# Performance work log

Measured on AMD Instinct MI355X. Metric: run time of the kernel, lower is better.

## Reference

```python
import jax, jax.numpy as jnp
import numpy as np

N = 100_000      # nodes
E = 1_600_000    # edges
NG = 512         # graphs in batch
EPS = 1e-5


def _prop(x, src, dst, n, add_self_loops):
    """GCN-normalized sparse propagation: agg_i = sum_{j->i} d_j^-1/2 d_i^-1/2 x_j."""
    ones = jnp.ones(src.shape[0], x.dtype)
    deg = jax.ops.segment_sum(ones, dst, num_segments=n)
    if add_self_loops:
        deg = deg + 1.0
    dinv = jnp.where(deg > 0, jax.lax.rsqrt(jnp.maximum(deg, 1e-12)), 0.0)
    w = dinv[src] * dinv[dst]                       # [E]
    agg = jax.ops.segment_sum(x[src] * w[:, None], dst, num_segments=n)
    if add_self_loops:
        agg = agg + x * (dinv * dinv)[:, None]
    return agg


def setup_inputs() -> dict:
    key = jax.random.key(0)
    ks = jax.random.split(key, 24)
    w = lambda k, s: jax.random.normal(k, s, jnp.float32) * 0.05
    dim = 100
    return {
        "x": jax.random.normal(ks[0], (N, 128), jnp.float32),
        "src": jax.random.randint(ks[1], (E,), 0, N),
        "dst": jax.random.randint(ks[2], (E,), 0, N),
        "batch": jnp.sort(jax.random.randint(ks[3], (N,), 0, NG)),
        # SGConv 1 & 2 (propagate then Linear)
        "W1": w(ks[4], (128, dim)), "b1": jnp.zeros((dim,), jnp.float32),
        "W2": w(ks[5], (dim, dim)), "b2": jnp.zeros((dim,), jnp.float32),
        # BatchNorm1d affine params
        "gamma": jnp.ones((dim,), jnp.float32), "beta": jnp.zeros((dim,), jnp.float32),
        # ARMAConv (num_stacks=1, num_layers=1)
        "Wa_init": w(ks[6], (dim, dim)), "Wa_root": w(ks[7], (dim, dim)),
        "ba": jnp.zeros((dim,), jnp.float32),
        # MLP head
        "Wf1": w(ks[8], (dim, 2 * dim)), "bf1": jnp.zeros((2 * dim,), jnp.float32),
        "Wf2": w(ks[9], (2 * dim, 3 * dim)), "bf2": jnp.zeros((3 * dim,), jnp.float32),
        "Wf3": w(ks[10], (3 * dim, 2 * dim)), "bf3": jnp.zeros((2 * dim,), jnp.float32),
        "Wf4": w(ks[11], (2 * dim, 1)), "bf4": jnp.zeros((1,), jnp.float32),
    }


def reference(x, src, dst, batch, W1, b1, W2, b2, gamma, beta,
              Wa_init, Wa_root, ba, Wf1, bf1, Wf2, bf2, Wf3, bf3, Wf4, bf4):
    n = x.shape[0]
    # SGConv (K=1): propagate with self-loop gcn_norm, then linear; ReLU
    h = jax.nn.relu(_prop(x, src, dst, n, True) @ W1 + b1)
    h = jax.nn.relu(_prop(h, src, dst, n, True) @ W2 + b2)
    # BatchNorm1d (training mode: batch statistics, biased var)
    mu = jnp.mean(h, axis=0)
    var = jnp.mean((h - mu) ** 2, axis=0)
    h = (h - mu) * jax.lax.rsqrt(var + EPS) * gamma + beta
    # ARMAConv (1 stack, 1 layer): ReLU(A_hat (h W_init) + h W_root + b), no self-loops
    a = jax.nn.relu(_prop(h @ Wa_init, src, dst, n, False) + h @ Wa_root + ba)
    # global_add_pool over graph ids
    g = jax.ops.segment_sum(a, batch, num_segments=NG)   # [NG, dim]
    # MLP head
    g = jax.nn.relu(g @ Wf1 + bf1)
    g = jax.nn.relu(g @ Wf2 + bf2)
    g = jax.nn.relu(g @ Wf3 + bf3)
    return g @ Wf4 + bf4
```

## Files before the change

kernel.cpp:

```cpp
#include <hip/hip_runtime.h>
#include <hip/hip_fp16.h>

#define NNODES 100000
#define NEDGES 1600000
#define NGRAPH 512
#define DIM    100
#define DP     128
#define EPSBN  1e-5f
#define NBUK   ((NNODES + 255) >> 8)
#define BINCH  2048

typedef _Float16 half8 __attribute__((ext_vector_type(8)));
typedef float floatx4 __attribute__((ext_vector_type(4)));

__global__ __launch_bounds__(512) void bin_count_kernel(const int* __restrict__ dst,
                                                        int* __restrict__ btotal, int e) {
    __shared__ int lc[NBUK];
    int tid = threadIdx.x;
    int base = blockIdx.x * BINCH;
    int m = e - base; if (m > BINCH) m = BINCH;
    for (int b = tid; b < NBUK; b += 512) lc[b] = 0;
    __syncthreads();
    for (int j = tid; j < m; j += 512)
        atomicAdd(&lc[dst[base + j] >> 8], 1);
    __syncthreads();
    for (int b = tid; b < NBUK; b += 512)
        if (lc[b]) atomicAdd(&btotal[b], lc[b]);
}

__global__ void bucket_scan_kernel(const int* __restrict__ btotal, int* __restrict__ bbase,
                                   int* __restrict__ bcursor, int e,
                                   const int* __restrict__ batch, int* __restrict__ gstart, int n) {
    __shared__ int s[512];
    int tid = threadIdx.x;
    int v = (tid < NBUK) ? btotal[tid] : 0;
    s[tid] = v; __syncthreads();
    for (int o = 1; o < 512; o <<= 1) {
        int t = (tid >= o) ? s[tid - o] : 0;
        __syncthreads();
        s[tid] += t;
        __syncthreads();
    }
    if (tid < NBUK) {
        int base = s[tid] - v;
        bbase[tid] = base;
        bcursor[tid] = base;
    }
    if (tid == 0) bbase[NBUK] = e;

    {
        int g = tid;
        int lo = 0, hi = n;
        while (lo < hi) {
            int mid = (lo + hi) >> 1;
            if (batch[mid] < g) lo = mid + 1; else hi = mid;
        }
        gstart[g] = lo;
        if (g == 0) gstart[NGRAPH] = n;
    }
}

__global__ __launch_bounds__(512) void bin_kernel(
        const int* __restrict__ src, const int* __restrict__ dst,
        int* __restrict__ bcursor, unsigned int* __restrict__ gpairs, int e) {
    __shared__ int2 lpairs[BINCH];
    __shared__ int lcount[NBUK], lstart[NBUK], lcur[NBUK], gbase[NBUK];
    __shared__ int s[512];
    int tid = threadIdx.x;
    int base = blockIdx.x * BINCH;
    int m = e - base; if (m > BINCH) m = BINCH;

    for (int b = tid; b < NBUK; b += 512) lcount[b] = 0;
    __syncthreads();
    for (int j = tid; j < m; j += 512)
        atomicAdd(&lcount[dst[base + j] >> 8], 1);
    __syncthreads();

    int v = (tid < NBUK) ? lcount[tid] : 0;
    s[tid] = v; __syncthreads();
    for (int o = 1; o < 512; o <<= 1) {
        int t = (tid >= o) ? s[tid - o] : 0;
        __syncthreads();
        s[tid] += t;
        __syncthreads();
    }
    if (tid < NBUK) {
        lstart[tid] = s[tid] - v;
        lcur[tid] = s[tid] - v;
        gbase[tid] = atomicAdd(&bcursor[tid], v);
    }
    __syncthreads();

    for (int j = tid; j < m; j += 512) {
        int sv = src[base + j], d = dst[base + j];
        int p = atomicAdd(&lcur[d >> 8], 1);
        lpairs[p] = make_int2(sv, d);
    }
    __syncthreads();
    for (int j = tid; j < m; j += 512) {
        int2 pr = lpairs[j];
        int b = pr.y >> 8;
        gpairs[gbase[b] + (j - lstart[b])] =
            ((unsigned int)pr.x << 8) | ((unsigned int)pr.y & 255u);
    }
}

__global__ __launch_bounds__(256) void bucket_build_kernel(
        const unsigned int* __restrict__ gpairs, const int* __restrict__ bbase,
        int* __restrict__ off, int* __restrict__ ssorted,
        float* __restrict__ dsl, float* __restrict__ dnsl, int n, int e) {
    __shared__ int cnt[256];
    __shared__ int sc[256];
    int b = blockIdx.x, tid = threadIdx.x;
    int node0 = b << 8;
    int e0 = bbase[b], e1 = bbase[b + 1];

    cnt[tid] = 0;
    __syncthreads();
    for (int j = e0 + tid; j < e1; j += 256)
        atomicAdd(&cnt[gpairs[j] & 255u], 1);
    __syncthreads();

    int c = cnt[tid];
    sc[tid] = c; __syncthreads();
    for (int o = 1; o < 256; o <<= 1) {
        int t = (tid >= o) ? sc[tid - o] : 0;
        __syncthreads();
        sc[tid] += t;
        __syncthreads();
    }
    int excl = sc[tid] - c;

    int node = node0 + tid;
    if (node < n) {
        off[node] = e0 + excl;
        float cf = (float)c;
        dsl[node] = rsqrtf(cf + 1.0f);
        dnsl[node] = (c > 0) ? rsqrtf(cf) : 0.0f;
    }
    if (b == NBUK - 1 && tid == 0) off[n] = e;

    __syncthreads();
    cnt[tid] = e0 + excl;
    __syncthreads();
    for (int j = e0 + tid; j < e1; j += 256) {
        unsigned int pk = gpairs[j];
        int p = atomicAdd(&cnt[pk & 255u], 1);
        ssorted[p] = (int)(pk >> 8);
    }
}

__global__ void packW4_kernel(const float* __restrict__ W1, const float* __restrict__ W2,
                              const float* __restrict__ W3, const float* __restrict__ W4,
                              _Float16* __restrict__ Wt1, _Float16* __restrict__ Wt2,
                              _Float16* __restrict__ Wt3, _Float16* __restrict__ Wt4,
                              const float* __restrict__ b1, const float* __restrict__ b2,
                              float* __restrict__ b1p, float* __restrict__ b2p,
                              int* __restrict__ btotal, float* __restrict__ bnsum,
                              float* __restrict__ bnsq, __half* __restrict__ buf0zr) {
    if (blockIdx.x == 256) {
        int t = threadIdx.x;
        if (t < 128) {
            b1p[t] = (t < DIM) ? b1[t] : 0.f;
            b2p[t] = (t < DIM) ? b2[t] : 0.f;
            bnsum[t] = 0.f;
            bnsq[t] = 0.f;
        }
        for (int i = t; i < NBUK; i += 256) btotal[i] = 0;
        if (t < 64) ((unsigned int*)buf0zr)[t] = 0u;
        return;
    }
    int which = blockIdx.x >> 6;
    int idx = (blockIdx.x & 63) * 256 + threadIdx.x;
    const float* W = (which == 0) ? W1 : (which == 1) ? W2 : (which == 2) ? W3 : W4;
    _Float16* Wt  = (which == 0) ? Wt1 : (which == 1) ? Wt2 : (which == 2) ? Wt3 : Wt4;
    int K = (which == 0) ? 128 : DIM;
    int j = idx & 7;
    int l = (idx >> 3) & 63;
    int c = idx >> 9;
    int t = c >> 2, k0 = c & 3;
    int nn = t * 16 + (l & 15);
    int k = k0 * 32 + (l >> 4) * 8 + j;
    float v = (k < K && nn < DIM) ? W[k * DIM + nn] : 0.f;
    Wt[idx] = (_Float16)v;
}

__global__ __launch_bounds__(256) void prop_kernel(
        const __half* __restrict__ pre, const int* __restrict__ ssorted,
        const int* __restrict__ off, const float* __restrict__ dinv,
        const float* __restrict__ bias, __half* __restrict__ outH, int n) {
    int wave = (blockIdx.x * blockDim.x + threadIdx.x) >> 6;
    int lane = threadIdx.x & 63;
    if (wave >= n) return;
    int e0 = off[wave], e1 = off[wave + 1];
    int deg = e1 - e0;
    int g = lane >> 4;
    int q = lane & 15;
    const int ZR = n;

    float acc[8];
#pragma unroll
    for (int i = 0; i < 8; i++) acc[i] = 0.f;

    auto addu = [&](uint4 u) {
        float2 f;
        f = __half22float2(*(__half2*)&u.x); acc[0] += f.x; acc[1] += f.y;
        f = __half22float2(*(__half2*)&u.y); acc[2] += f.x; acc[3] += f.y;
        f = __half22float2(*(__half2*)&u.z); acc[4] += f.x; acc[5] += f.y;
        f = __half22float2(*(__half2*)&u.w); acc[6] += f.x; acc[7] += f.y;
    };
    auto rowptr = [&](int s) -> const uint4* {
        return (const uint4*)&pre[(long)s * DP + q * 8];
    };

    for (int base = 0; base < deg; base += 64) {
        int m = deg - base; if (m > 64) m = 64;
        int sidx = (lane < m) ? ssorted[e0 + base + lane] : ZR;
        for (int j = 0; j < m; j += 16) {
            int s0 = __shfl(sidx, j + g);
            int s1 = __shfl(sidx, j + 4 + g);
            int s2 = __shfl(sidx, j + 8 + g);
            int s3 = __shfl(sidx, j + 12 + g);
            uint4 u0 = *rowptr(s0);
            uint4 u1 = *rowptr(s1);
            uint4 u2 = *rowptr(s2);
            uint4 u3 = *rowptr(s3);
            addu(u0); addu(u1); addu(u2); addu(u3);
        }
    }

#pragma unroll
    for (int i = 0; i < 8; i++) {
        acc[i] += __shfl_xor(acc[i], 16);
        acc[i] += __shfl_xor(acc[i], 32);
    }

    if (g == 0) {
        float dn = dinv[wave];
        addu(*rowptr(wave));
        float4 b0 = *(const float4*)&bias[q * 8];
        float4 b1v = *(const float4*)&bias[q * 8 + 4];
        float o[8];
        o[0] = fmaxf(dn * acc[0] + b0.x, 0.f);
        o[1] = fmaxf(dn * acc[1] + b0.y, 0.f);
        o[2] = fmaxf(dn * acc[2] + b0.z, 0.f);
        o[3] = fmaxf(dn * acc[3] + b0.w, 0.f);
        o[4] = fmaxf(dn * acc[4] + b1v.x, 0.f);
        o[5] = fmaxf(dn * acc[5] + b1v.y, 0.f);
        o[6] = fmaxf(dn * acc[6] + b1v.z, 0.f);
        o[7] = fmaxf(dn * acc[7] + b1v.w, 0.f);
        __half2 p0 = __floats2half2_rn(o[0], o[1]);
        __half2 p1 = __floats2half2_rn(o[2], o[3]);
        __half2 p2 = __floats2half2_rn(o[4], o[5]);
        __half2 p3 = __floats2half2_rn(o[6], o[7]);
        uint4 u;
        u.x = *(unsigned int*)&p0;
        u.y = *(unsigned int*)&p1;
        u.z = *(unsigned int*)&p2;
        u.w = *(unsigned int*)&p3;
        *(uint4*)&outH[(long)wave * DP + q * 8] = u;
    }
}

__global__ __launch_bounds__(256) void prop_arma_kernel(
        const __half* __restrict__ pre, const int* __restrict__ ssorted,
        const int* __restrict__ off, const float* __restrict__ dinv,
        const __half* __restrict__ R, __half* __restrict__ outH, int n) {
    int wave = (blockIdx.x * blockDim.x + threadIdx.x) >> 6;
    int lane = threadIdx.x & 63;
    if (wave >= n) return;
    int e0 = off[wave], e1 = off[wave + 1];
    int deg = e1 - e0;
    int g = lane >> 4;
    int q = lane & 15;
    const int ZR = n;

    float acc[8];
#pragma unroll
    for (int i = 0; i < 8; i++) acc[i] = 0.f;

    auto addu = [&](uint4 u) {
        float2 f;
        f = __half22float2(*(__half2*)&u.x); acc[0] += f.x; acc[1] += f.y;
        f = __half22float2(*(__half2*)&u.y); acc[2] += f.x; acc[3] += f.y;
        f = __half22float2(*(__half2*)&u.z); acc[4] += f.x; acc[5] += f.y;
        f = __half22float2(*(__half2*)&u.w); acc[6] += f.x; acc[7] += f.y;
    };
    auto rowptr = [&](int s) -> const uint4* {
        return (const uint4*)&pre[(long)s * DP + q * 8];
    };

    for (int base = 0; base < deg; base += 64) {
        int m = deg - base; if (m > 64) m = 64;
        int sidx = (lane < m) ? ssorted[e0 + base + lane] : ZR;
        for (int j = 0; j < m; j += 16) {
            int s0 = __shfl(sidx, j + g);
            int s1 = __shfl(sidx, j + 4 + g);
            int s2 = __shfl(sidx, j + 8 + g);
            int s3 = __shfl(sidx, j + 12 + g);
            uint4 u0 = *rowptr(s0);
            uint4 u1 = *rowptr(s1);
            uint4 u2 = *rowptr(s2);
            uint4 u3 = *rowptr(s3);
            addu(u0); addu(u1); addu(u2); addu(u3);
        }
    }

#pragma unroll
    for (int i = 0; i < 8; i++) {
        acc[i] += __shfl_xor(acc[i], 16);
        acc[i] += __shfl_xor(acc[i], 32);
    }

    if (g == 0) {
        float dn = dinv[wave];
        uint4 r4 = *(const uint4*)&R[(long)wave * DP + q * 8];
        float rr[8];
        float2 f;
        f = __half22float2(*(__half2*)&r4.x); rr[0] = f.x; rr[1] = f.y;
        f = __half22float2(*(__half2*)&r4.y); rr[2] = f.x; rr[3] = f.y;
        f = __half22float2(*(__half2*)&r4.z); rr[4] = f.x; rr[5] = f.y;
        f = __half22float2(*(__half2*)&r4.w); rr[6] = f.x; rr[7] = f.y;
        float o[8];
#pragma unroll
        for (int i = 0; i < 8; i++) o[i] = fmaxf(dn * acc[i] + rr[i], 0.f);
        __half2 p0 = __floats2half2_rn(o[0], o[1]);
        __half2 p1 = __floats2half2_rn(o[2], o[3]);
        __half2 p2 = __floats2half2_rn(o[4], o[5]);
        __half2 p3 = __floats2half2_rn(o[6], o[7]);
        uint4 u;
        u.x = *(unsigned int*)&p0;
        u.y = *(unsigned int*)&p1;
        u.z = *(unsigned int*)&p2;
        u.w = *(unsigned int*)&p3;
        *(uint4*)&outH[(long)wave * DP + q * 8] = u;
    }
}

__global__ __launch_bounds__(256) void matmul_a32_kernel(
        const float* __restrict__ A, const _Float16* __restrict__ WtF,
        const float* __restrict__ rowscale, __half* __restrict__ Ch, int M) {
    __shared__ char smraw[64 * 132 * 4];
    _Float16* Bs = (_Float16*)smraw;
    float* Ct = (float*)smraw;
    int tid = threadIdx.x;
    int wave = tid >> 6;
    int lane = tid & 63;
    int m16 = lane & 15;
    int quad = lane >> 4;
    long row0blk = (long)blockIdx.x * 128;

    {
        const uint4* s = (const uint4*)WtF;
        uint4* d = (uint4*)Bs;
        for (int i = tid; i < 2048; i += 256) d[i] = s[i];
    }

    half8 af[2][4];
#pragma unroll
    for (int t = 0; t < 2; t++) {
        long ar = row0blk + t * 64 + wave * 16 + m16; if (ar >= M) ar = M - 1;
        const float* Ap = &A[ar * DP + quad * 8];
#pragma unroll
        for (int k0 = 0; k0 < 4; k0++) {
            float4 v0 = *(const float4*)(Ap + k0 * 32);
            float4 v1 = *(const float4*)(Ap + k0 * 32 + 4);
            half8 o;
            o[0] = (_Float16)v0.x; o[1] = (_Float16)v0.y;
            o[2] = (_Float16)v0.z; o[3] = (_Float16)v0.w;
            o[4] = (_Float16)v1.x; o[5] = (_Float16)v1.y;
            o[6] = (_Float16)v1.z; o[7] = (_Float16)v1.w;
            af[t][k0] = o;
        }
    }
    __syncthreads();

    floatx4 acc[2][8];
#pragma unroll
    for (int t = 0; t < 2; t++)
#pragma unroll
        for (int a = 0; a < 8; a++) acc[t][a] = (floatx4){0.f, 0.f, 0.f, 0.f};

#pragma unroll
    for (int c = 0; c < 32; c++) {
        half8 bf = *(const half8*)&Bs[(c * 64 + lane) * 8];
        acc[0][c >> 2] = __builtin_amdgcn_mfma_f32_16x16x32_f16(af[0][c & 3], bf, acc[0][c >> 2], 0, 0, 0);
        acc[1][c >> 2] = __builtin_amdgcn_mfma_f32_16x16x32_f16(af[1][c & 3], bf, acc[1][c >> 2], 0, 0, 0);
    }

    int lrow0 = wave * 16 + quad * 4;
#pragma unroll
    for (int t = 0; t < 2; t++) {
        __syncthreads();
#pragma unroll
        for (int a = 0; a < 8; a++)
#pragma unroll
            for (int r = 0; r < 4; r++)
                Ct[(lrow0 + r) * 132 + a * 16 + m16] = acc[t][a][r];
        __syncthreads();
        for (int idx = tid; idx < 64 * 32; idx += 256) {
            int lr = idx >> 5, c4 = idx & 31;
            long grow = row0blk + t * 64 + lr;
            if (grow >= M) continue;
            int col = c4 * 4;
            float4 v = *(const float4*)&Ct[lr * 132 + col];
            float rs = rowscale[grow];
            v.x *= rs; v.y *= rs; v.z *= rs; v.w *= rs;
            __half2 p01 = __floats2half2_rn(v.x, v.y);
            __half2 p23 = __floats2half2_rn(v.z, v.w);
            uint2 u;
            u.x = *(unsigned int*)&p01;
            u.y = *(unsigned int*)&p23;
            *(uint2*)&Ch[grow * DP + col] = u;
        }
    }
}

__global__ __launch_bounds__(256) void matmul_a16_kernel(
        const __half* __restrict__ A, const _Float16* __restrict__ WtF,
        const float* __restrict__ rowscale, __half* __restrict__ Ch, int M) {
    __shared__ char smraw[64 * 132 * 4];
    _Float16* Bs = (_Float16*)smraw;
    float* Ct = (float*)smraw;
    int tid = threadIdx.x;
    int wave = tid >> 6;
    int lane = tid & 63;
    int m16 = lane & 15;
    int quad = lane >> 4;
    long row0blk = (long)blockIdx.x * 128;

    {
        const uint4* s = (const uint4*)WtF;
        uint4* d = (uint4*)Bs;
        for (int i = tid; i < 2048; i += 256) d[i] = s[i];
    }

    half8 af[2][4];
#pragma unroll
    for (int t = 0; t < 2; t++) {
        long ar = row0blk + t * 64 + wave * 16 + m16; if (ar >= M) ar = M - 1;
        const _Float16* Ap = (const _Float16*)&A[ar * DP + quad * 8];
#pragma unroll
        for (int k0 = 0; k0 < 4; k0++)
            af[t][k0] = *(const half8*)(Ap + k0 * 32);
    }
    __syncthreads();

    floatx4 acc[2][8];
#pragma unroll
    for (int t = 0; t < 2; t++)
#pragma unroll
        for (int a = 0; a < 8; a++) acc[t][a] = (floatx4){0.f, 0.f, 0.f, 0.f};

#pragma unroll
    for (int c = 0; c < 32; c++) {
        half8 bf = *(const half8*)&Bs[(c * 64 + lane) * 8];
        acc[0][c >> 2] = __builtin_amdgcn_mfma_f32_16x16x32_f16(af[0][c & 3], bf, acc[0][c >> 2], 0, 0, 0);
        acc[1][c >> 2] = __builtin_amdgcn_mfma_f32_16x16x32_f16(af[1][c & 3], bf, acc[1][c >> 2], 0, 0, 0);
    }

    int lrow0 = wave * 16 + quad * 4;
#pragma unroll
    for (int t = 0; t < 2; t++) {
        __syncthreads();
#pragma unroll
        for (int a = 0; a < 8; a++)
#pragma unroll
            for (int r = 0; r < 4; r++)
                Ct[(lrow0 + r) * 132 + a * 16 + m16] = acc[t][a][r];
        __syncthreads();
        for (int idx = tid; idx < 64 * 32; idx += 256) {
            int lr = idx >> 5, c4 = idx & 31;
            long grow = row0blk + t * 64 + lr;
            if (grow >= M) continue;
            int col = c4 * 4;
            float4 v = *(const float4*)&Ct[lr * 132 + col];
            float rs = rowscale[grow];
            v.x *= rs; v.y *= rs; v.z *= rs; v.w *= rs;
            __half2 p01 = __floats2half2_rn(v.x, v.y);
            __half2 p23 = __floats2half2_rn(v.z, v.w);
            uint2 u;
            u.x = *(unsigned int*)&p01;
            u.y = *(unsigned int*)&p23;
            *(uint2*)&Ch[grow * DP + col] = u;
        }
    }
}

__global__ __launch_bounds__(256) void matmul_dual_kernel(
        const __half* __restrict__ A, const _Float16* __restrict__ WtF3,
        const _Float16* __restrict__ WtF4, const float* __restrict__ ba,
        const float* __restrict__ rowscale,
        const float* __restrict__ bnscale, const float* __restrict__ bnshift,
        __half* __restrict__ Ch1, __half* __restrict__ ChR, int M, int Kout) {
    __shared__ char smraw[64 * 132 * 4];
    _Float16* Bs = (_Float16*)smraw;
    float* Ct = (float*)smraw;
    int tid = threadIdx.x;
    int wave = tid >> 6;
    int lane = tid & 63;
    int m16 = lane & 15;
    int quad = lane >> 4;
    long row0blk = (long)blockIdx.x * 64;
    long row0 = row0blk + wave * 16;

    half8 af[4];
    {
        long ar = row0 + m16; if (ar >= M) ar = M - 1;
        const _Float16* Ap = (const _Float16*)&A[ar * DP + quad * 8];
#pragma unroll
        for (int k0 = 0; k0 < 4; k0++) {
            half8 h = *(const half8*)(Ap + k0 * 32);
            int c0 = quad * 8 + k0 * 32;
            float4 sc0 = *(const float4*)&bnscale[c0];
            float4 sc1 = *(const float4*)&bnscale[c0 + 4];
            float4 sh0 = *(const float4*)&bnshift[c0];
            float4 sh1 = *(const float4*)&bnshift[c0 + 4];
            half8 o;
            o[0] = (_Float16)((float)h[0] * sc0.x + sh0.x);
            o[1] = (_Float16)((float)h[1] * sc0.y + sh0.y);
            o[2] = (_Float16)((float)h[2] * sc0.z + sh0.z);
            o[3] = (_Float16)((float)h[3] * sc0.w + sh0.w);
            o[4] = (_Float16)((float)h[4] * sc1.x + sh1.x);
            o[5] = (_Float16)((float)h[5] * sc1.y + sh1.y);
            o[6] = (_Float16)((float)h[6] * sc1.z + sh1.z);
            o[7] = (_Float16)((float)h[7] * sc1.w + sh1.w);
            af[k0] = o;
        }
    }

    floatx4 acc3[8], acc4[8];
#pragma unroll
    for (int t = 0; t < 8; t++) {
        acc3[t] = (floatx4){0.f, 0.f, 0.f, 0.f};
        acc4[t] = (floatx4){0.f, 0.f, 0.f, 0.f};
    }

    {
        const uint4* s = (const uint4*)WtF3;
        uint4* d = (uint4*)Bs;
        for (int i = tid; i < 2048; i += 256) d[i] = s[i];
    }
    __syncthreads();
#pragma unroll
    for (int c = 0; c < 32; c++) {
        half8 bf = *(const half8*)&Bs[(c * 64 + lane) * 8];
        acc3[c >> 2] = __builtin_amdgcn_mfma_f32_16x16x32_f16(af[c & 3], bf, acc3[c >> 2], 0, 0, 0);
    }
    __syncthreads();

    {
        const uint4* s = (const uint4*)WtF4;
        uint4* d = (uint4*)Bs;
        for (int i = tid; i < 2048; i += 256) d[i] = s[i];
    }
    __syncthreads();
#pragma unroll
    for (int c = 0; c < 32; c++) {
        half8 bf = *(const half8*)&Bs[(c * 64 + lane) * 8];
        acc4[c >> 2] = __builtin_amdgcn_mfma_f32_16x16x32_f16(af[c & 3], bf, acc4[c >> 2], 0, 0, 0);
    }
    __syncthreads();

    int lrow0 = wave * 16 + quad * 4;

#pragma unroll
    for (int t = 0; t < 8; t++)
#pragma unroll
        for (int r = 0; r < 4; r++)
            Ct[(lrow0 + r) * 132 + t * 16 + m16] = acc3[t][r];
    __syncthreads();
    for (int idx = tid; idx < 64 * 32; idx += 256) {
        int lr = idx >> 5, c4 = idx & 31;
        long grow = row0blk + lr;
        if (grow >= M) continue;
        int col = c4 * 4;
        float4 v = *(const float4*)&Ct[lr * 132 + col];
        float rs = rowscale[grow];
        v.x *= rs; v.y *= rs; v.z *= rs; v.w *= rs;
        __half2 p01 = __floats2half2_rn(v.x, v.y);
        __half2 p23 = __floats2half2_rn(v.z, v.w);
        uint2 u;
        u.x = *(unsigned int*)&p01;
        u.y = *(unsigned int*)&p23;
        *(uint2*)&Ch1[grow * DP + col] = u;
    }
    __syncthreads();

#pragma unroll
    for (int t = 0; t < 8; t++)
#pragma unroll
        for (int r = 0; r < 4; r++)
            Ct[(lrow0 + r) * 132 + t * 16 + m16] = acc4[t][r];
    __syncthreads();
    for (int idx = tid; idx < 64 * 32; idx += 256) {
        int lr = idx >> 5, c4 = idx & 31;
        long grow = row0blk + lr;
        if (grow >= M) continue;
        int col = c4 * 4;
        float4 v = *(const float4*)&Ct[lr * 132 + col];
        if (col + 4 <= Kout) {
            float4 bb = *(const float4*)&ba[col];
            v.x += bb.x; v.y += bb.y; v.z += bb.z; v.w += bb.w;
        }
        __half2 p01 = __floats2half2_rn(v.x, v.y);
        __half2 p23 = __floats2half2_rn(v.z, v.w);
        uint2 u;
        u.x = *(unsigned int*)&p01;
        u.y = *(unsigned int*)&p23;
        *(uint2*)&ChR[grow * DP + col] = u;
    }
}

__global__ __launch_bounds__(512) void bnstats_kernel(const __half* __restrict__ h,
                                                      float* __restrict__ bnsum,
                                                      float* __restrict__ bnsq, int n) {
    __shared__ float2 sred[512], qred[512];
    int tid = threadIdx.x;
    int col2 = tid & 63;
    int rgrp = tid >> 6;
    float2 s = make_float2(0.f, 0.f), qv = make_float2(0.f, 0.f);
    if (col2 < 52) {
        for (int r = blockIdx.x * 8 + rgrp; r < n; r += gridDim.x * 8) {
            __half2 hv = *(const __half2*)&h[(long)r * DP + col2 * 2];
            float2 f = __half22float2(hv);
            s.x += f.x; s.y += f.y;
            qv.x += f.x * f.x; qv.y += f.y * f.y;
        }
    }
    sred[tid] = s; qred[tid] = qv;
    __syncthreads();
    if (tid < 52) {
        float2 ts = make_float2(0.f, 0.f), tq = make_float2(0.f, 0.f);
#pragma unroll
        for (int gg = 0; gg < 8; gg++) {
            float2 v = sred[gg * 64 + tid]; ts.x += v.x; ts.y += v.y;
            v = qred[gg * 64 + tid]; tq.x += v.x; tq.y += v.y;
        }
        atomicAdd(&bnsum[tid * 2], ts.x);
        atomicAdd(&bnsum[tid * 2 + 1], ts.y);
        atomicAdd(&bnsq[tid * 2], tq.x);
        atomicAdd(&bnsq[tid * 2 + 1], tq.y);
    }
}

__global__ void bn_prep_kernel(const float* __restrict__ sum, const float* __restrict__ sq,
                               const float* __restrict__ gamma, const float* __restrict__ beta,
                               float* __restrict__ scale, float* __restrict__ shift, int n) {
    int c = threadIdx.x;
    float sc = 0.f, sh = 0.f;
    if (c < DIM) {
        float inv_n = 1.0f / (float)n;
        float mu = sum[c] * inv_n;
        float var = sq[c] * inv_n - mu * mu;
        float rs = rsqrtf(var + EPSBN);
        sc = rs * gamma[c];
        sh = beta[c] - mu * sc;
    }
    scale[c] = sc;
    shift[c] = sh;
}

__global__ __launch_bounds__(512) void pmlp_kernel(
        const __half* __restrict__ a, const int* __restrict__ gstart,
        const float* __restrict__ Wf1, const float* __restrict__ bf1,
        const float* __restrict__ Wf2, const float* __restrict__ bf2,
        const float* __restrict__ Wf3, const float* __restrict__ bf3,
        const float* __restrict__ Wf4, const float* __restrict__ bf4,
        float* __restrict__ out) {
    __shared__ float2 red[512];
    __shared__ float gsum[128], a1[200], a2[300], a3[200], red1[512];
    int b = blockIdx.x, tid = threadIdx.x;

    {
        int col2 = tid & 63;
        int rgrp = tid >> 6;
        int lo = gstart[b], hi = gstart[b + 1];
        float2 s = make_float2(0.f, 0.f);
        for (int r = lo + rgrp; r < hi; r += 8) {
            __half2 h = *(const __half2*)&a[(long)r * DP + col2 * 2];
            float2 f = __half22float2(h);
            s.x += f.x; s.y += f.y;
        }
        red[tid] = s;
        __syncthreads();
        if (tid < 64) {
            float2 t = make_float2(0.f, 0.f);
#pragma unroll
            for (int gg = 0; gg < 8; gg++) {
                float2 v = red[gg * 64 + tid];
                t.x += v.x; t.y += v.y;
            }
            gsum[tid * 2] = t.x;
            gsum[tid * 2 + 1] = t.y;
        }
        __syncthreads();
    }

    for (int c = tid; c < 200; c += 512) {
        float s = bf1[c];
        for (int k = 0; k < 100; k++) s += gsum[k] * Wf1[k * 200 + c];
        a1[c] = fmaxf(s, 0.f);
    }
    __syncthreads();
    for (int c = tid; c < 300; c += 512) {
        float s = bf2[c];
        for (int k = 0; k < 200; k++) s += a1[k] * Wf2[k * 300 + c];
        a2[c] = fmaxf(s, 0.f);
    }
    __syncthreads();
    for (int c = tid; c < 200; c += 512) {
        float s = bf3[c];
        for (int k = 0; k < 300; k++) s += a2[k] * Wf3[k * 200 + c];
        a3[c] = fmaxf(s, 0.f);
    }
    __syncthreads();
    red1[tid] = (tid < 200) ? a3[tid] * Wf4[tid] : 0.f;
    __syncthreads();
    for (int o = 256; o > 0; o >>= 1) {
        if (tid < o) red1[tid] += red1[tid + o];
        __syncthreads();
    }
    if (tid == 0) out[b] = red1[0] + bf4[0];
}

extern "C" void kernel_launch(void* const* d_in, const int* in_sizes, int n_in,
                              void* d_out, int out_size, void* d_ws, size_t ws_size,
                              hipStream_t stream) {
    const float* x      = (const float*)d_in[0];
    const int*   src    = (const int*)d_in[1];
    const int*   dst    = (const int*)d_in[2];
    const int*   batch  = (const int*)d_in[3];
    const float* W1     = (const float*)d_in[4];
    const float* b1     = (const float*)d_in[5];
    const float* W2     = (const float*)d_in[6];
    const float* b2     = (const float*)d_in[7];
    const float* gamma  = (const float*)d_in[8];
    const float* beta   = (const float*)d_in[9];
    const float* Wa_init= (const float*)d_in[10];
    const float* Wa_root= (const float*)d_in[11];
    const float* ba     = (const float*)d_in[12];
    const float* Wf1    = (const float*)d_in[13];
    const float* bf1    = (const float*)d_in[14];
    const float* Wf2    = (const float*)d_in[15];
    const float* bf2    = (const float*)d_in[16];
    const float* Wf3    = (const float*)d_in[17];
    const float* bf3    = (const float*)d_in[18];
    const float* Wf4    = (const float*)d_in[19];
    const float* bf4    = (const float*)d_in[20];
    float* out = (float*)d_out;

    const int n = NNODES;
    const int e = NEDGES;

    char* ws = (char*)d_ws;
    auto carve = [&](size_t bytes) -> void* {
        void* p = (void*)ws;
        ws += (bytes + 255) & ~(size_t)255;
        return p;
    };
    __half* buf0    = (__half*)carve((size_t)(n + 1) * DP * 2);
    __half* buf1    = (__half*)carve((size_t)n * DP * 2);
    __half* bufR    = (__half*)carve((size_t)n * DP * 2);
    __half* bufC    = (__half*)carve((size_t)n * DP * 2);
    _Float16* Wt1   = (_Float16*)carve((size_t)DP * DP * 2);
    _Float16* Wt2   = (_Float16*)carve((size_t)DP * DP * 2);
    _Float16* Wt3   = (_Float16*)carve((size_t)DP * DP * 2);
    _Float16* Wt4   = (_Float16*)carve((size_t)DP * DP * 2);
    int*    off     = (int*)carve((size_t)(n + 1) * 4);
    int*    btotal  = (int*)carve((size_t)NBUK * 4);
    int*    bbase   = (int*)carve((size_t)(NBUK + 1) * 4);
    int*    bcursor = (int*)carve((size_t)NBUK * 4);
    int*    ssorted = (int*)carve((size_t)e * 4);
    unsigned int* gpairs = (unsigned int*)carve((size_t)e * 4);
    float*  dinv_sl = (float*)carve((size_t)n * 4);
    float*  dinv_nsl= (float*)carve((size_t)n * 4);
    float*  bnsum   = (float*)carve(DP * 4);
    float*  bnsq    = (float*)carve(DP * 4);
    float*  bnscale = (float*)carve(DP * 4);
    float*  bnshift = (float*)carve(DP * 4);
    float*  b1p     = (float*)carve(DP * 4);
    float*  b2p     = (float*)carve(DP * 4);
    int*    gstart  = (int*)carve((size_t)(NGRAPH + 1) * 4);

    const int nchunk = (e + BINCH - 1) / BINCH;

    packW4_kernel<<<257, 256, 0, stream>>>(W1, W2, Wa_init, Wa_root, Wt1, Wt2, Wt3, Wt4,
                                           b1, b2, b1p, b2p, btotal, bnsum, bnsq,
                                           buf0 + (size_t)n * DP);

    bin_count_kernel<<<nchunk, 512, 0, stream>>>(dst, btotal, e);
    bucket_scan_kernel<<<1, 512, 0, stream>>>(btotal, bbase, bcursor, e, batch, gstart, n);
    bin_kernel<<<nchunk, 512, 0, stream>>>(src, dst, bcursor, gpairs, e);
    bucket_build_kernel<<<NBUK, 256, 0, stream>>>(gpairs, bbase, off, ssorted, dinv_sl, dinv_nsl, n, e);

    const int prop_blocks = (n + 3) / 4;
    const int mm_blocks128 = (n + 127) / 128;
    const int mm_blocks64 = (n + 63) / 64;

    matmul_a32_kernel<<<mm_blocks128, 256, 0, stream>>>(x, Wt1, dinv_sl, buf0, n);
    prop_kernel<<<prop_blocks, 256, 0, stream>>>(buf0, ssorted, off, dinv_sl, b1p, buf1, n);

    matmul_a16_kernel<<<mm_blocks128, 256, 0, stream>>>(buf1, Wt2, dinv_sl, buf0, n);
    prop_kernel<<<prop_blocks, 256, 0, stream>>>(buf0, ssorted, off, dinv_sl, b2p, buf1, n);

    bnstats_kernel<<<512, 512, 0, stream>>>(buf1, bnsum, bnsq, n);
    bn_prep_kernel<<<1, 128, 0, stream>>>(bnsum, bnsq, gamma, beta, bnscale, bnshift, n);

    matmul_dual_kernel<<<mm_blocks64, 256, 0, stream>>>(buf1, Wt3, Wt4, ba, dinv_nsl, bnscale, bnshift, buf0, bufR, n, DIM);
    prop_arma_kernel<<<prop_blocks, 256, 0, stream>>>(buf0, ssorted, off, dinv_nsl, bufR, bufC, n);

    pmlp_kernel<<<NGRAPH, 512, 0, stream>>>(bufC, gstart, Wf1, bf1, Wf2, bf2, Wf3, bf3, Wf4, bf4, out);
}
```

Before: 504.5 us.

## Slice propagation features into per-XCD column slabs with work-stealing queues

The pre-propagation matmul output now goes into 7 column slices of 16 halves each, rather than a 128-wide padded row layout. The three propagation kernels are merged into one persistent kernel. Each block picks a slice based on its XCC id and pulls 128-node chunks from an atomic queue, stealing from other slices once its own queue is empty. The aim is to keep each slice's 3.2MB gather footprint resident in one XCD's L2 and to stop gathering padded columns, at the cost of atomic queue traffic and the assumption that there are 7-8 XCDs.

```diff
diff --git a/kernel.cpp b/kernel.cpp
--- a/kernel.cpp
+++ b/kernel.cpp
@@ -6,12 +6,17 @@
 #define NGRAPH 512
 #define DIM    100
 #define DP     128
+#define SLICES 7
 #define EPSBN  1e-5f
 #define NBUK   ((NNODES + 255) >> 8)
 #define BINCH  2048
+#define PERW   32
+#define NCH    128
+#define QPAD   32
 
 typedef _Float16 half8 __attribute__((ext_vector_type(8)));
 typedef float floatx4 __attribute__((ext_vector_type(4)));
+
 
 __global__ __launch_bounds__(512) void bin_count_kernel(const int* __restrict__ dst,
                                                         int* __restrict__ btotal, int e) {
@@ -157,7 +162,8 @@
                               const float* __restrict__ b1, const float* __restrict__ b2,
                               float* __restrict__ b1p, float* __restrict__ b2p,
                               int* __restrict__ btotal, float* __restrict__ bnsum,
-                              float* __restrict__ bnsq, __half* __restrict__ buf0zr) {
+                              float* __restrict__ bnsq, __half* __restrict__ buf0,
+                              int* __restrict__ qcur, int n) {
     if (blockIdx.x == 256) {
         int t = threadIdx.x;
         if (t < 128) {
@@ -167,7 +173,11 @@
             bnsq[t] = 0.f;
         }
         for (int i = t; i < NBUK; i += 256) btotal[i] = 0;
-        if (t < 64) ((unsigned int*)buf0zr)[t] = 0u;
+        for (int i = t; i < 3 * SLICES * QPAD; i += 256) qcur[i] = 0;
+        if (t < SLICES * 8) {
+            int sl = t >> 3, wd = t & 7;
+            ((unsigned int*)buf0)[((size_t)sl * (n + 1) + n) * 8 + wd] = 0u;
+        }
         return;
     }
     int which = blockIdx.x >> 6;
@@ -185,155 +195,148 @@
     Wt[idx] = (_Float16)v;
 }
 
-__global__ __launch_bounds__(256) void prop_kernel(
-        const __half* __restrict__ pre, const int* __restrict__ ssorted,
+__global__ __launch_bounds__(256) void prop_slice_kernel(
+        const __half* __restrict__ T, const int* __restrict__ ssorted,
         const int* __restrict__ off, const float* __restrict__ dinv,
-        const float* __restrict__ bias, __half* __restrict__ outH, int n) {
-    int wave = (blockIdx.x * blockDim.x + threadIdx.x) >> 6;
-    int lane = threadIdx.x & 63;
-    if (wave >= n) return;
-    int e0 = off[wave], e1 = off[wave + 1];
-    int deg = e1 - e0;
-    int g = lane >> 4;
-    int q = lane & 15;
+        const float* __restrict__ bias, const __half* __restrict__ R,
+        __half* __restrict__ outH, int* __restrict__ qcur, int n, int nchunks) {
+    __shared__ int sh_sc;
+    int tid = threadIdx.x;
+    int lane = tid & 63;
+    int w = tid >> 6;
+    int half = lane >> 5;
+    int p2 = lane & 31;
     const int ZR = n;
 
-    float acc[8];
-#pragma unroll
-    for (int i = 0; i < 8; i++) acc[i] = 0.f;
-
-    auto addu = [&](uint4 u) {
-        float2 f;
-        f = __half22float2(*(__half2*)&u.x); acc[0] += f.x; acc[1] += f.y;
-        f = __half22float2(*(__half2*)&u.y); acc[2] += f.x; acc[3] += f.y;
-        f = __half22float2(*(__half2*)&u.z); acc[4] += f.x; acc[5] += f.y;
-        f = __half22float2(*(__half2*)&u.w); acc[6] += f.x; acc[7] += f.y;
-    };
-    auto rowptr = [&](int s) -> const uint4* {
-        return (const uint4*)&pre[(long)s * DP + q * 8];
-    };
-
-    for (int base = 0; base < deg; base += 64) {
-        int m = deg - base; if (m > 64) m = 64;
-        int sidx = (lane < m) ? ssorted[e0 + base + lane] : ZR;
-        for (int j = 0; j < m; j += 16) {
-            int s0 = __shfl(sidx, j + g);
-            int s1 = __shfl(sidx, j + 4 + g);
-            int s2 = __shfl(sidx, j + 8 + g);
-            int s3 = __shfl(sidx, j + 12 + g);
-            uint4 u0 = *rowptr(s0);
-            uint4 u1 = *rowptr(s1);
-            uint4 u2 = *rowptr(s2);
-            uint4 u3 = *rowptr(s3);
-            addu(u0); addu(u1); addu(u2); addu(u3);
-        }
-    }
-
-#pragma unroll
-    for (int i = 0; i < 8; i++) {
-        acc[i] += __shfl_xor(acc[i], 16);
-        acc[i] += __shfl_xor(acc[i], 32);
-    }
-
-    if (g == 0) {
-        float dn = dinv[wave];
-        addu(*rowptr(wave));
-        float4 b0 = *(const float4*)&bias[q * 8];
-        float4 b1v = *(const float4*)&bias[q * 8 + 4];
-        float o[8];
-        o[0] = fmaxf(dn * acc[0] + b0.x, 0.f);
-        o[1] = fmaxf(dn * acc[1] + b0.y, 0.f);
-        o[2] = fmaxf(dn * acc[2] + b0.z, 0.f);
-        o[3] = fmaxf(dn * acc[3] + b0.w, 0.f);
-        o[4] = fmaxf(dn * acc[4] + b1v.x, 0.f);
-        o[5] = fmaxf(dn * acc[5] + b1v.y, 0.f);
-        o[6] = fmaxf(dn * acc[6] + b1v.z, 0.f);
-        o[7] = fmaxf(dn * acc[7] + b1v.w, 0.f);
-        __half2 p0 = __floats2half2_rn(o[0], o[1]);
-        __half2 p1 = __floats2half2_rn(o[2], o[3]);
-        __half2 p2 = __floats2half2_rn(o[4], o[5]);
-        __half2 p3 = __floats2half2_rn(o[6], o[7]);
-        uint4 u;
-        u.x = *(unsigned int*)&p0;
-        u.y = *(unsigned int*)&p1;
-        u.z = *(unsigned int*)&p2;
-        u.w = *(unsigned int*)&p3;
-        *(uint4*)&outH[(long)wave * DP + q * 8] = u;
-    }
-}
-
-__global__ __launch_bounds__(256) void prop_arma_kernel(
-        const __half* __restrict__ pre, const int* __restrict__ ssorted,
-        const int* __restrict__ off, const float* __restrict__ dinv,
-        const __half* __restrict__ R, __half* __restrict__ outH, int n) {
-    int wave = (blockIdx.x * blockDim.x + threadIdx.x) >> 6;
-    int lane = threadIdx.x & 63;
-    if (wave >= n) return;
-    int e0 = off[wave], e1 = off[wave + 1];
-    int deg = e1 - e0;
-    int g = lane >> 4;
-    int q = lane & 15;
-    const int ZR = n;
-
-    float acc[8];
-#pragma unroll
-    for (int i = 0; i < 8; i++) acc[i] = 0.f;
-
-    auto addu = [&](uint4 u) {
-        float2 f;
-        f = __half22float2(*(__half2*)&u.x); acc[0] += f.x; acc[1] += f.y;
-        f = __half22float2(*(__half2*)&u.y); acc[2] += f.x; acc[3] += f.y;
-        f = __half22float2(*(__half2*)&u.z); acc[4] += f.x; acc[5] += f.y;
-        f = __half22float2(*(__half2*)&u.w); acc[6] += f.x; acc[7] += f.y;
-    };
-    auto rowptr = [&](int s) -> const uint4* {
-        return (const uint4*)&pre[(long)s * DP + q * 8];
-    };
-
-    for (int base = 0; base < deg; base += 64) {
-        int m = deg - base; if (m > 64) m = 64;
-        int sidx = (lane < m) ? ssorted[e0 + base + lane] : ZR;
-        for (int j = 0; j < m; j += 16) {
-            int s0 = __shfl(sidx, j + g);
-            int s1 = __shfl(sidx, j + 4 + g);
-            int s2 = __shfl(sidx, j + 8 + g);
-            int s3 = __shfl(sidx, j + 12 + g);
-            uint4 u0 = *rowptr(s0);
-            uint4 u1 = *rowptr(s1);
-            uint4 u2 = *rowptr(s2);
-            uint4 u3 = *rowptr(s3);
-            addu(u0); addu(u1); addu(u2); addu(u3);
-        }
-    }
-
-#pragma unroll
-    for (int i = 0; i < 8; i++) {
-        acc[i] += __shfl_xor(acc[i], 16);
-        acc[i] += __shfl_xor(acc[i], 32);
-    }
-
-    if (g == 0) {
-        float dn = dinv[wave];
-        uint4 r4 = *(const uint4*)&R[(long)wave * DP + q * 8];
-        float rr[8];
-        float2 f;
-        f = __half22float2(*(__half2*)&r4.x); rr[0] = f.x; rr[1] = f.y;
-        f = __half22float2(*(__half2*)&r4.y); rr[2] = f.x; rr[3] = f.y;
-        f = __half22float2(*(__half2*)&r4.z); rr[4] = f.x; rr[5] = f.y;
-        f = __half22float2(*(__half2*)&r4.w); rr[6] = f.x; rr[7] = f.y;
-        float o[8];
-#pragma unroll
-        for (int i = 0; i < 8; i++) o[i] = fmaxf(dn * acc[i] + rr[i], 0.f);
-        __half2 p0 = __floats2half2_rn(o[0], o[1]);
-        __half2 p1 = __floats2half2_rn(o[2], o[3]);
-        __half2 p2 = __floats2half2_rn(o[4], o[5]);
-        __half2 p3 = __floats2half2_rn(o[6], o[7]);
-        uint4 u;
-        u.x = *(unsigned int*)&p0;
-        u.y = *(unsigned int*)&p1;
-        u.z = *(unsigned int*)&p2;
-        u.w = *(unsigned int*)&p3;
-        *(uint4*)&outH[(long)wave * DP + q * 8] = u;
+    int s0;
+    {
+        unsigned xcc = __builtin_amdgcn_s_getreg(0xF814) & 15u;
+        s0 = (int)(xcc & 7u); if (s0 > 6) s0 = 6;
+    }
+
+    while (true) {
+        if (tid == 0) {
+            int got = -1;
+            int c = atomicAdd(&qcur[s0 * QPAD], 1);
+            if (c < nchunks) got = (s0 << 16) | c;
+            else {
+                for (int t = 1; t <= 6 && got < 0; t++) {
+                    int ss = s0 + t; if (ss > 6) ss -= 7;
+                    int cc = atomicAdd(&qcur[ss * QPAD], 1);
+                    if (cc < nchunks) got = (ss << 16) | cc;
+                }
+            }
+            sh_sc = got;
+        }
+        __syncthreads();
+        int enc = sh_sc;
+        __syncthreads();
+        if (enc < 0) return;
+        int s = enc >> 16;
+        int chunk = enc & 0xFFFF;
+        const __half* Ts = T + (size_t)s * (n + 1) * 16;
+        int nb = chunk * NCH + w * PERW;
+
+        for (int i = 0; i < PERW; i += 2) {
+            int va = nb + i, vb = nb + i + 1;
+            if (va >= n) break;
+            bool haveB = (vb < n);
+            int e0a = off[va], e1a = off[va + 1];
+            int e0b = haveB ? off[vb] : 0, e1b = haveB ? off[vb + 1] : 0;
+            int e0h = half ? e0b : e0a;
+            int degh = half ? (e1b - e0b) : (e1a - e0a);
+
+            float fa[16];
+#pragma unroll
+            for (int j2 = 0; j2 < 16; j2++) fa[j2] = 0.f;
+
+            for (int base = 0; base < degh; base += 32) {
+                int sidx = (base + p2 < degh) ?
+                    __builtin_nontemporal_load(&ssorted[e0h + base + p2]) : ZR;
+                const uint4* p = (const uint4*)&Ts[(size_t)sidx * 16];
+                uint4 u0 = p[0];
+                uint4 u1 = p[1];
+                float2 f;
+                f = __half22float2(*(__half2*)&u0.x); fa[0] += f.x;  fa[1] += f.y;
+                f = __half22float2(*(__half2*)&u0.y); fa[2] += f.x;  fa[3] += f.y;
+                f = __half22float2(*(__half2*)&u0.z); fa[4] += f.x;  fa[5] += f.y;
+                f = __half22float2(*(__half2*)&u0.w); fa[6] += f.x;  fa[7] += f.y;
+                f = __half22float2(*(__half2*)&u1.x); fa[8] += f.x;  fa[9] += f.y;
+                f = __half22float2(*(__half2*)&u1.y); fa[10] += f.x; fa[11] += f.y;
+                f = __half22float2(*(__half2*)&u1.z); fa[12] += f.x; fa[13] += f.y;
+                f = __half22float2(*(__half2*)&u1.w); fa[14] += f.x; fa[15] += f.y;
+            }
+
+#pragma unroll
+            for (int j2 = 0; j2 < 16; j2++) {
+                fa[j2] += __shfl_xor(fa[j2], 1);
+                fa[j2] += __shfl_xor(fa[j2], 2);
+                fa[j2] += __shfl_xor(fa[j2], 4);
+                fa[j2] += __shfl_xor(fa[j2], 8);
+                fa[j2] += __shfl_xor(fa[j2], 16);
+            }
+
+            int v = half ? vb : va;
+            bool act = (p2 < 2) && (half == 0 || haveB);
+            if (act) {
+                float v0 = p2 ? fa[8]  : fa[0];
+                float v1 = p2 ? fa[9]  : fa[1];
+                float v2 = p2 ? fa[10] : fa[2];
+                float v3 = p2 ? fa[11] : fa[3];
+                float v4 = p2 ? fa[12] : fa[4];
+                float v5 = p2 ? fa[13] : fa[5];
+                float v6 = p2 ? fa[14] : fa[6];
+                float v7 = p2 ? fa[15] : fa[7];
+                float dn = dinv[v];
+                float o[8];
+                if (bias) {
+                    const uint4* sp = (const uint4*)&Ts[(size_t)v * 16];
+                    uint4 su = sp[p2];
+                    float2 f;
+                    float sf0, sf1, sf2, sf3, sf4, sf5, sf6, sf7;
+                    f = __half22float2(*(__half2*)&su.x); sf0 = f.x; sf1 = f.y;
+                    f = __half22float2(*(__half2*)&su.y); sf2 = f.x; sf3 = f.y;
+                    f = __half22float2(*(__half2*)&su.z); sf4 = f.x; sf5 = f.y;
+                    f = __half22float2(*(__half2*)&su.w); sf6 = f.x; sf7 = f.y;
+                    float4 bA = *(const float4*)&bias[s * 16 + p2 * 8];
+                    float4 bB = *(const float4*)&bias[s * 16 + p2 * 8 + 4];
+                    o[0] = fmaxf(dn * (v0 + sf0) + bA.x, 0.f);
+                    o[1] = fmaxf(dn * (v1 + sf1) + bA.y, 0.f);
+                    o[2] = fmaxf(dn * (v2 + sf2) + bA.z, 0.f);
+                    o[3] = fmaxf(dn * (v3 + sf3) + bA.w, 0.f);
+                    o[4] = fmaxf(dn * (v4 + sf4) + bB.x, 0.f);
+                    o[5] = fmaxf(dn * (v5 + sf5) + bB.y, 0.f);
+                    o[6] = fmaxf(dn * (v6 + sf6) + bB.z, 0.f);
+                    o[7] = fmaxf(dn * (v7 + sf7) + bB.w, 0.f);
+                } else {
+                    uint4 ru = *(const uint4*)&R[(size_t)v * DP + s * 16 + p2 * 8];
+                    float2 f;
+                    float rf0, rf1, rf2, rf3, rf4, rf5, rf6, rf7;
+                    f = __half22float2(*(__half2*)&ru.x); rf0 = f.x; rf1 = f.y;
+                    f = __half22float2(*(__half2*)&ru.y); rf2 = f.x; rf3 = f.y;
+                    f = __half22float2(*(__half2*)&ru.z); rf4 = f.x; rf5 = f.y;
+                    f = __half22float2(*(__half2*)&ru.w); rf6 = f.x; rf7 = f.y;
+                    o[0] = fmaxf(dn * v0 + rf0, 0.f);
+                    o[1] = fmaxf(dn * v1 + rf1, 0.f);
+                    o[2] = fmaxf(dn * v2 + rf2, 0.f);
+                    o[3] = fmaxf(dn * v3 + rf3, 0.f);
+                    o[4] = fmaxf(dn * v4 + rf4, 0.f);
+                    o[5] = fmaxf(dn * v5 + rf5, 0.f);
+                    o[6] = fmaxf(dn * v6 + rf6, 0.f);
+                    o[7] = fmaxf(dn * v7 + rf7, 0.f);
+                }
+                __half2 q0 = __floats2half2_rn(o[0], o[1]);
+                __half2 q1 = __floats2half2_rn(o[2], o[3]);
+                __half2 q2 = __floats2half2_rn(o[4], o[5]);
+                __half2 q3 = __floats2half2_rn(o[6], o[7]);
+                uint4 u;
+                u.x = *(unsigned int*)&q0;
+                u.y = *(unsigned int*)&q1;
+                u.z = *(unsigned int*)&q2;
+                u.w = *(unsigned int*)&q3;
+                *(uint4*)&outH[(size_t)v * DP + s * 16 + p2 * 8] = u;
+            }
+        }
     }
 }
 
@@ -401,8 +404,8 @@
         for (int idx = tid; idx < 64 * 32; idx += 256) {
             int lr = idx >> 5, c4 = idx & 31;
             long grow = row0blk + t * 64 + lr;
-            if (grow >= M) continue;
             int col = c4 * 4;
+            if (grow >= M || col >= SLICES * 16) continue;
             float4 v = *(const float4*)&Ct[lr * 132 + col];
             float rs = rowscale[grow];
             v.x *= rs; v.y *= rs; v.z *= rs; v.w *= rs;
@@ -411,7 +414,7 @@
             uint2 u;
             u.x = *(unsigned int*)&p01;
             u.y = *(unsigned int*)&p23;
-            *(uint2*)&Ch[grow * DP + col] = u;
+            *(uint2*)&Ch[((size_t)(col >> 4) * (M + 1) + grow) * 16 + (col & 15)] = u;
         }
     }
 }
@@ -472,8 +475,8 @@
         for (int idx = tid; idx < 64 * 32; idx += 256) {
             int lr = idx >> 5, c4 = idx & 31;
             long grow = row0blk + t * 64 + lr;
-            if (grow >= M) continue;
             int col = c4 * 4;
+            if (grow >= M || col >= SLICES * 16) continue;
             float4 v = *(const float4*)&Ct[lr * 132 + col];
             float rs = rowscale[grow];
             v.x *= rs; v.y *= rs; v.z *= rs; v.w *= rs;
@@ -482,7 +485,7 @@
             uint2 u;
             u.x = *(unsigned int*)&p01;
             u.y = *(unsigned int*)&p23;
-            *(uint2*)&Ch[grow * DP + col] = u;
+            *(uint2*)&Ch[((size_t)(col >> 4) * (M + 1) + grow) * 16 + (col & 15)] = u;
         }
     }
 }
@@ -573,8 +576,8 @@
     for (int idx = tid; idx < 64 * 32; idx += 256) {
         int lr = idx >> 5, c4 = idx & 31;
         long grow = row0blk + lr;
-        if (grow >= M) continue;
         int col = c4 * 4;
+        if (grow >= M || col >= SLICES * 16) continue;
         float4 v = *(const float4*)&Ct[lr * 132 + col];
         float rs = rowscale[grow];
         v.x *= rs; v.y *= rs; v.z *= rs; v.w *= rs;
@@ -583,7 +586,7 @@
         uint2 u;
         u.x = *(unsigned int*)&p01;
         u.y = *(unsigned int*)&p23;
-        *(uint2*)&Ch1[grow * DP + col] = u;
+        *(uint2*)&Ch1[((size_t)(col >> 4) * (M + 1) + grow) * 16 + (col & 15)] = u;
     }
     __syncthreads();
 
@@ -759,7 +762,7 @@
         ws += (bytes + 255) & ~(size_t)255;
         return p;
     };
-    __half* buf0    = (__half*)carve((size_t)(n + 1) * DP * 2);
+    __half* buf0    = (__half*)carve((size_t)SLICES * (n + 1) * 16 * 2);
     __half* buf1    = (__half*)carve((size_t)n * DP * 2);
     __half* bufR    = (__half*)carve((size_t)n * DP * 2);
     __half* bufC    = (__half*)carve((size_t)n * DP * 2);
@@ -781,34 +784,36 @@
     float*  bnshift = (float*)carve(DP * 4);
     float*  b1p     = (float*)carve(DP * 4);
     float*  b2p     = (float*)carve(DP * 4);
+    int*    qcur    = (int*)carve((size_t)3 * SLICES * QPAD * 4);
     int*    gstart  = (int*)carve((size_t)(NGRAPH + 1) * 4);
 
     const int nchunk = (e + BINCH - 1) / BINCH;
+    const int nchunks = (n + NCH - 1) / NCH;
+    const int prop_grid = 2048;
 
     packW4_kernel<<<257, 256, 0, stream>>>(W1, W2, Wa_init, Wa_root, Wt1, Wt2, Wt3, Wt4,
                                            b1, b2, b1p, b2p, btotal, bnsum, bnsq,
-                                           buf0 + (size_t)n * DP);
+                                           buf0, qcur, n);
 
     bin_count_kernel<<<nchunk, 512, 0, stream>>>(dst, btotal, e);
     bucket_scan_kernel<<<1, 512, 0, stream>>>(btotal, bbase, bcursor, e, batch, gstart, n);
     bin_kernel<<<nchunk, 512, 0, stream>>>(src, dst, bcursor, gpairs, e);
     bucket_build_kernel<<<NBUK, 256, 0, stream>>>(gpairs, bbase, off, ssorted, dinv_sl, dinv_nsl, n, e);
 
-    const int prop_blocks = (n + 3) / 4;
     const int mm_blocks128 = (n + 127) / 128;
     const int mm_blocks64 = (n + 63) / 64;
 
     matmul_a32_kernel<<<mm_blocks128, 256, 0, stream>>>(x, Wt1, dinv_sl, buf0, n);
-    prop_kernel<<<prop_blocks, 256, 0, stream>>>(buf0, ssorted, off, dinv_sl, b1p, buf1, n);
+    prop_slice_kernel<<<prop_grid, 256, 0, stream>>>(buf0, ssorted, off, dinv_sl, b1p, nullptr, buf1, qcur, n, nchunks);
 
     matmul_a16_kernel<<<mm_blocks128, 256, 0, stream>>>(buf1, Wt2, dinv_sl, buf0, n);
-    prop_kernel<<<prop_blocks, 256, 0, stream>>>(buf0, ssorted, off, dinv_sl, b2p, buf1, n);
+    prop_slice_kernel<<<prop_grid, 256, 0, stream>>>(buf0, ssorted, off, dinv_sl, b2p, nullptr, buf1, qcur + SLICES * QPAD, n, nchunks);
 
     bnstats_kernel<<<512, 512, 0, stream>>>(buf1, bnsum, bnsq, n);
     bn_prep_kernel<<<1, 128, 0, stream>>>(bnsum, bnsq, gamma, beta, bnscale, bnshift, n);
 
     matmul_dual_kernel<<<mm_blocks64, 256, 0, stream>>>(buf1, Wt3, Wt4, ba, dinv_nsl, bnscale, bnshift, buf0, bufR, n, DIM);
-    prop_arma_kernel<<<prop_blocks, 256, 0, stream>>>(buf0, ssorted, off, dinv_nsl, bufR, bufC, n);
+    prop_slice_kernel<<<prop_grid, 256, 0, stream>>>(buf0, ssorted, off, dinv_nsl, nullptr, bufR, bufC, qcur + 2 * SLICES * QPAD, n, nchunks);
 
     pmlp_kernel<<<NGRAPH, 512, 0, stream>>>(bufC, gstart, Wf1, bf1, Wf2, bf2, Wf3, bf3, Wf4, bf4, out);
 }
```

Measured after the change: 1.260 ms. 2.5x slower.
